# Kernel optimization log

Hardware: AMD Instinct MI355X
Metric: run time of the kernel (lower is better)

## Reference

```python
import jax, jax.numpy as jnp
import numpy as np

USR_SIZE = 100000
EMB = 64
BATCH = 4096
HIST = 200


def setup_inputs() -> dict:
    key = jax.random.key(0)
    k1, k2 = jax.random.split(key)
    # USERLIST as stored by the module: np.append(-1, param.USERLIST), sorted ids
    userlist = jnp.concatenate([jnp.array([-1], dtype=jnp.int64),
                                jnp.arange(USR_SIZE, dtype=jnp.int64)])
    x = jax.random.randint(k1, (BATCH, HIST), 0, USR_SIZE, dtype=jnp.int64)
    emb_usr = jax.random.normal(k2, (USR_SIZE + 1, EMB), dtype=jnp.float32)
    return {"x": x, "userlist": userlist, "emb_usr": emb_usr}


def reference(x, userlist, emb_usr):
    # Equivalent to per-element np.where(USERLIST == u)[0][0]: USERLIST is
    # sorted and every u appears exactly once, so searchsorted gives the
    # same index as the linear scan. Then a single embedding gather.
    usr2id = jnp.searchsorted(userlist, x)  # [B, L]
    return emb_usr[usr2id]                  # [B, L, EMB]
```

## Files before the change

kernel.cpp:

```cpp
#include <hip/hip_runtime.h>
#include <hip/hip_bf16.h>


#define ELEMS_PER_BLOCK 256
#define V4_PER_ROW 16

__global__ __launch_bounds__(256) void usr_emb_gather(
    const int* __restrict__ x,
    const int* __restrict__ userlist, int n_user,
    const float* __restrict__ emb,
    float* __restrict__ out,
    int n_elem)
{
    __shared__ int s_id[ELEMS_PER_BLOCK];

    const int t    = threadIdx.x;
    const int base = blockIdx.x * ELEMS_PER_BLOCK;

    {
        const int e = base + t;
        if (e < n_elem) {
            const int u = x[e];
            int lo = 0, hi = n_user;
            while (lo < hi) {
                const int mid = (lo + hi) >> 1;
                if (userlist[mid] < u) lo = mid + 1;
                else                   hi = mid;
            }
            s_id[t] = lo;
        }
    }
    __syncthreads();

    const float4* __restrict__ emb4 = (const float4*)emb;
    float4*       __restrict__ out4 = (float4*)out;

    const int sub  = t & (V4_PER_ROW - 1);
    const int eoff = t >> 4;

#pragma unroll
    for (int iter = 0; iter < ELEMS_PER_BLOCK / 16; ++iter) {
        const int local_e = eoff + iter * 16;
        const int ge      = base + local_e;
        if (ge < n_elem) {
            const int id = s_id[local_e];
            out4[(size_t)ge * V4_PER_ROW + sub] = emb4[(size_t)id * V4_PER_ROW + sub];
        }
    }
}

extern "C" void kernel_launch(void* const* d_in, const int* in_sizes, int n_in,
                              void* d_out, int out_size, void* d_ws, size_t ws_size,
                              hipStream_t stream) {
    const int*   x        = (const int*)d_in[0];
    const int*   userlist = (const int*)d_in[1];
    const float* emb      = (const float*)d_in[2];
    float*       out      = (float*)d_out;

    const int n_elem = in_sizes[0];
    const int n_user = in_sizes[1];

    const int blocks = (n_elem + ELEMS_PER_BLOCK - 1) / ELEMS_PER_BLOCK;
    usr_emb_gather<<<blocks, 256, 0, stream>>>(x, userlist, n_user, emb, out, n_elem);
}
```

Measured before the change: 274.8 us.

## Guess user index directly with verified fallback and share ids via wave shuffles

Each thread first guesses the index from the offset of its id relative to userlist[1] and checks that one entry. It falls back to the full binary search only when the check fails, so a contiguous sorted list skips the chain of dependent search loads. The shared-memory id buffer and block barrier are replaced by per-wavefront __shfl broadcasts, so each 64-lane wave gathers its own 64 rows independently. Non-contiguous user lists still take the binary-search path, now with one extra load per element.

```diff
diff --git a/kernel.cpp b/kernel.cpp
--- a/kernel.cpp
+++ b/kernel.cpp
@@ -2,7 +2,6 @@
 #include <hip/hip_bf16.h>
 
 
-#define ELEMS_PER_BLOCK 256
 #define V4_PER_ROW 16
 
 __global__ __launch_bounds__(256) void usr_emb_gather(
@@ -12,38 +11,47 @@
     float* __restrict__ out,
     int n_elem)
 {
-    __shared__ int s_id[ELEMS_PER_BLOCK];
+    const int t      = threadIdx.x;
+    const int lane   = t & 63;
+    const int wave   = t >> 6;
+    const int wbase  = blockIdx.x * 256 + wave * 64;
 
-    const int t    = threadIdx.x;
-    const int base = blockIdx.x * ELEMS_PER_BLOCK;
-
+    int my_id = 0;
     {
-        const int e = base + t;
+        const int e = wbase + lane;
         if (e < n_elem) {
-            const int u = x[e];
-            int lo = 0, hi = n_user;
-            while (lo < hi) {
-                const int mid = (lo + hi) >> 1;
-                if (userlist[mid] < u) lo = mid + 1;
-                else                   hi = mid;
+            const int u  = x[e];
+            const int v1 = userlist[1];
+            int g = 1 + (u - v1);
+            bool hit = false;
+            if (g >= 1 && g < n_user) {
+                hit = (userlist[g] == u);
             }
-            s_id[t] = lo;
+            if (!hit) {
+                int lo = 0, hi = n_user;
+                while (lo < hi) {
+                    const int mid = (lo + hi) >> 1;
+                    if (userlist[mid] < u) lo = mid + 1;
+                    else                   hi = mid;
+                }
+                g = lo;
+            }
+            my_id = g;
         }
     }
-    __syncthreads();
 
     const float4* __restrict__ emb4 = (const float4*)emb;
     float4*       __restrict__ out4 = (float4*)out;
 
-    const int sub  = t & (V4_PER_ROW - 1);
-    const int eoff = t >> 4;
+    const int sub   = lane & (V4_PER_ROW - 1);
+    const int eslot = lane >> 4;
 
 #pragma unroll
-    for (int iter = 0; iter < ELEMS_PER_BLOCK / 16; ++iter) {
-        const int local_e = eoff + iter * 16;
-        const int ge      = base + local_e;
+    for (int iter = 0; iter < 16; ++iter) {
+        const int local = eslot + iter * 4;
+        const int id    = __shfl(my_id, local);
+        const int ge    = wbase + local;
         if (ge < n_elem) {
-            const int id = s_id[local_e];
             out4[(size_t)ge * V4_PER_ROW + sub] = emb4[(size_t)id * V4_PER_ROW + sub];
         }
     }
@@ -60,6 +68,6 @@
     const int n_elem = in_sizes[0];
     const int n_user = in_sizes[1];
 
-    const int blocks = (n_elem + ELEMS_PER_BLOCK - 1) / ELEMS_PER_BLOCK;
+    const int blocks = (n_elem + 255) / 256;
     usr_emb_gather<<<blocks, 256, 0, stream>>>(x, userlist, n_user, emb, out, n_elem);
 }
```

After: 248.6 us. -9.5%, faster.
